# Kernel tuning notes

Measured on AMD Instinct MI355X. Metric: run time of the kernel, lower is better.

Reference implementation:

```python
import jax, jax.numpy as jnp
import numpy as np

N = 50000          # num nodes
E = 800000         # num edges (avg degree 16)
D_IN = 128         # input_size
H = 128            # hidden_size
BN_EPS = 1e-5


def setup_inputs() -> dict:
    key = jax.random.key(0)
    ks = jax.random.split(key, 16)
    std = 1.0 / np.sqrt(H)
    u = lambda k, shape: jax.random.uniform(k, shape, jnp.float32, -std, std)
    return {
        "x": jax.random.normal(ks[0], (N, D_IN), jnp.float32),
        "hx": jax.random.normal(ks[1], (N, H), jnp.float32),
        "cx": jax.random.normal(ks[2], (N, H), jnp.float32),
        "edge_src": jax.random.randint(ks[3], (E,), 0, N, jnp.int32),
        "edge_dst": jax.random.randint(ks[4], (E,), 0, N, jnp.int32),
        "edge_weight": jax.random.uniform(ks[5], (E,), jnp.float32) / 16.0,  # ~normalized adj values
        "gcn_weight": u(ks[6], (D_IN, H)),
        "bias": u(ks[7], (H,)),
        "x2h_w": u(ks[8], (4 * H, H)),
        "x2h_b": u(ks[9], (4 * H,)),
        "h2h_w": u(ks[10], (4 * H, H)),
        "h2h_b": u(ks[11], (4 * H,)),
        "bn_gamma": u(ks[12], (H,)),
        "bn_beta": u(ks[13], (H,)),
        "bn_mean": jnp.zeros((H,), jnp.float32),
        "bn_var": jnp.ones((H,), jnp.float32),
    }


def reference(x, hx, cx, edge_src, edge_dst, edge_weight, gcn_weight, bias,
              x2h_w, x2h_b, h2h_w, h2h_b, bn_gamma, bn_beta, bn_mean, bn_var):
    # GCN: support = x @ W, then sparse adj @ support via gather/segment-sum
    support = x @ gcn_weight                                   # (N, H)
    msgs = edge_weight[:, None] * support[edge_src]            # (E, H)
    agg = jax.ops.segment_sum(msgs, edge_dst, num_segments=N)  # (N, H) = spmm(adj, support)
    h = jax.nn.relu(agg)
    # dropout: eval mode -> identity
    h = h + bias
    # BatchNorm1d (eval mode, running stats)
    h = (h - bn_mean) * jax.lax.rsqrt(bn_var + BN_EPS) * bn_gamma + bn_beta
    # fused LSTM gates: x2h(h) + h2h(hx)
    gates = h @ x2h_w.T + x2h_b + hx @ h2h_w.T + h2h_b         # (N, 4H)
    i_g, f_g, g_g, o_g = jnp.split(gates, 4, axis=1)
    cy = cx * jax.nn.sigmoid(f_g) + jax.nn.sigmoid(i_g) * jnp.tanh(g_g)
    hy = jax.nn.sigmoid(o_g) * jnp.tanh(cy)
    return hy, cy
```

## Files before the change

kernel.cpp:

```cpp
#include <hip/hip_runtime.h>

#define NN 50000
#define NE 800000
#define HH 128
#define BN_EPS 1e-5f
#define SCAN_NB ((NN + 255) / 256)

typedef unsigned short u16;
typedef unsigned int u32;
typedef short bf16x8 __attribute__((ext_vector_type(8)));
typedef float f32x4 __attribute__((ext_vector_type(4)));

static __device__ __forceinline__ float bf2f(u16 u){
  union { u32 i; float f; } v; v.i = ((u32)u) << 16; return v.f;
}
static __device__ __forceinline__ u16 f2bf(float f){
  union { float f; u32 i; } v; v.f = f;
  u32 x = v.i;
  return (u16)((x + 0x7fffu + ((x >> 16) & 1u)) >> 16);
}
static __device__ __forceinline__ float sigm(float x){
  return 1.f / (1.f + __expf(-x));
}
static __device__ __forceinline__ float tanh_fast(float x){
  return 1.f - 2.f / (1.f + __expf(2.f * x));
}


__global__ void zero_kernel(int* __restrict__ p, int n){
  int i = blockIdx.x * blockDim.x + threadIdx.x;
  if (i < n) p[i] = 0;
}

__global__ void hist_kernel(const int* __restrict__ dst, int* __restrict__ counts, int E){
  int e = blockIdx.x * blockDim.x + threadIdx.x;
  if (e < E) atomicAdd(&counts[dst[e]], 1);
}


__global__ __launch_bounds__(256) void scan_bsum(
    const int* __restrict__ counts, int* __restrict__ bsums, int n){
  int i = blockIdx.x * 256 + threadIdx.x;
  int v = (i < n) ? counts[i] : 0;
#pragma unroll
  for (int off = 1; off < 64; off <<= 1) v += __shfl_xor(v, off);
  __shared__ int ws[4];
  if ((threadIdx.x & 63) == 0) ws[threadIdx.x >> 6] = v;
  __syncthreads();
  if (threadIdx.x == 0) bsums[blockIdx.x] = ws[0] + ws[1] + ws[2] + ws[3];
}

__global__ __launch_bounds__(256) void scan_tops(int* __restrict__ bsums, int nb){
  __shared__ int sh[256];
  int t = threadIdx.x;
  int v = (t < nb) ? bsums[t] : 0;
  sh[t] = v;
  __syncthreads();
  for (int off = 1; off < 256; off <<= 1){
    int u = (t >= off) ? sh[t - off] : 0;
    __syncthreads();
    sh[t] += u;
    __syncthreads();
  }
  if (t < nb) bsums[t] = sh[t] - v;
}

__global__ __launch_bounds__(256) void scan_final(
    const int* __restrict__ counts, const int* __restrict__ bsums,
    int* __restrict__ offs, int* __restrict__ cursor, int n){
  __shared__ int sh[256];
  int t = threadIdx.x;
  int i = blockIdx.x * 256 + t;
  int v = (i < n) ? counts[i] : 0;
  sh[t] = v;
  __syncthreads();
  for (int off = 1; off < 256; off <<= 1){
    int u = (t >= off) ? sh[t - off] : 0;
    __syncthreads();
    sh[t] += u;
    __syncthreads();
  }
  int excl = sh[t] - v + bsums[blockIdx.x];
  if (i < n){ offs[i] = excl; cursor[i] = excl; }
}

__global__ void scatter_kernel(const int* __restrict__ src, const int* __restrict__ dst,
                               const float* __restrict__ w, int* __restrict__ cursor,
                               int2* __restrict__ esw, int E){
  int e = blockIdx.x * blockDim.x + threadIdx.x;
  if (e < E){
    int d = dst[e];
    int pos = atomicAdd(&cursor[d], 1);
    esw[pos] = make_int2(src[e], __float_as_int(w[e]));
  }
}


__global__ void prep_pack(const float* __restrict__ x2hw, const float* __restrict__ h2hw,
                          const float* __restrict__ x2hb, const float* __restrict__ h2hb,
                          const float* __restrict__ gcnw,
                          u16* __restrict__ wcat, u16* __restrict__ wgcn,
                          float* __restrict__ bsum){
  int i = blockIdx.x * blockDim.x + threadIdx.x;
  int n = i >> 8, k = i & 255;
  float v = (k < 128) ? x2hw[n * 128 + k] : h2hw[n * 128 + (k - 128)];
  wcat[i] = f2bf(v);
  if (i < 16384){
    int nn = i >> 7, kk = i & 127;
    wgcn[i] = f2bf(gcnw[kk * 128 + nn]);
  }
  if (i < 512) bsum[i] = x2hb[i] + h2hb[i];
}

__global__ __launch_bounds__(256) void support_mfma(
    const float* __restrict__ x, const u16* __restrict__ wgcn,
    u16* __restrict__ support, int N){
  int tid = threadIdx.x;
  int wave = tid >> 6, lane = tid & 63;
  int c = lane & 15, q = lane >> 4;
  int row0 = blockIdx.x * 64 + wave * 16;
  int arow = row0 + c; if (arow > N - 1) arow = N - 1;
  f32x4 acc[8];
#pragma unroll
  for (int t = 0; t < 8; t++) acc[t] = (f32x4){0.f, 0.f, 0.f, 0.f};

  const u16* wp = wgcn + (size_t)c * 128 + q * 8;
#pragma unroll
  for (int k0 = 0; k0 < 128; k0 += 32){
    const float* ap = x + (size_t)arow * 128 + k0 + q * 8;
    float4 f0 = *(const float4*)ap;
    float4 f1 = *(const float4*)(ap + 4);
    u16 tmp[8] = {f2bf(f0.x), f2bf(f0.y), f2bf(f0.z), f2bf(f0.w),
                  f2bf(f1.x), f2bf(f1.y), f2bf(f1.z), f2bf(f1.w)};
    bf16x8 afrag = *(bf16x8*)tmp;
#pragma unroll
    for (int t = 0; t < 8; t++){
      bf16x8 bfrag = *(const bf16x8*)(wp + (size_t)t * 16 * 128 + k0);
      acc[t] = __builtin_amdgcn_mfma_f32_16x16x32_bf16(afrag, bfrag, acc[t], 0, 0, 0);
    }
  }
#pragma unroll
  for (int t = 0; t < 8; t++){
#pragma unroll
    for (int j = 0; j < 4; j++){
      int r = row0 + q * 4 + j;
      if (r < N) support[(size_t)r * 128 + t * 16 + c] = f2bf(acc[t][j]);
    }
  }
}

__global__ __launch_bounds__(256) void agg_bn2(
    const u16* __restrict__ support, const int2* __restrict__ esw,
    const int* __restrict__ offs, const int* __restrict__ counts,
    const float* __restrict__ bias, const float* __restrict__ gamma,
    const float* __restrict__ beta, const float* __restrict__ mean,
    const float* __restrict__ var, const float* __restrict__ hx,
    u16* __restrict__ hbn, u16* __restrict__ hxb, int N){
  int wid = blockIdx.x * 4 + (threadIdx.x >> 6);
  int lane = threadIdx.x & 63;
  if (wid >= N) return;
  int c = lane * 2;
  float2 hv = *(const float2*)(hx + (size_t)wid * HH + c);
  int start = offs[wid];
  int deg   = counts[wid];
  float a0 = 0.f, a1 = 0.f;
  for (int base = 0; base < deg; base += 64){
    int cnt = deg - base; if (cnt > 64) cnt = 64;
    int2 my = make_int2(0, 0);
    if (lane < cnt) my = esw[start + base + lane];
    int e = 0;
    for (; e + 8 <= cnt; e += 8){
      int s[8]; float g[8]; u32 u[8];
#pragma unroll
      for (int k = 0; k < 8; k++){
        s[k] = __shfl(my.x, e + k);
        g[k] = __int_as_float(__shfl(my.y, e + k));
      }
#pragma unroll
      for (int k = 0; k < 8; k++)
        u[k] = *(const u32*)(support + (size_t)s[k] * HH + c);
#pragma unroll
      for (int k = 0; k < 8; k++){
        a0 = fmaf(g[k], bf2f((u16)(u[k] & 0xffffu)), a0);
        a1 = fmaf(g[k], bf2f((u16)(u[k] >> 16)), a1);
      }
    }
    for (; e + 4 <= cnt; e += 4){
      int s[4]; float g[4]; u32 u[4];
#pragma unroll
      for (int k = 0; k < 4; k++){
        s[k] = __shfl(my.x, e + k);
        g[k] = __int_as_float(__shfl(my.y, e + k));
      }
#pragma unroll
      for (int k = 0; k < 4; k++)
        u[k] = *(const u32*)(support + (size_t)s[k] * HH + c);
#pragma unroll
      for (int k = 0; k < 4; k++){
        a0 = fmaf(g[k], bf2f((u16)(u[k] & 0xffffu)), a0);
        a1 = fmaf(g[k], bf2f((u16)(u[k] >> 16)), a1);
      }
    }
    for (; e < cnt; e++){
      int   si = __shfl(my.x, e);
      float gi = __int_as_float(__shfl(my.y, e));
      u32 ui = *(const u32*)(support + (size_t)si * HH + c);
      a0 = fmaf(gi, bf2f((u16)(ui & 0xffffu)), a0);
      a1 = fmaf(gi, bf2f((u16)(ui >> 16)), a1);
    }
  }
  float h0 = fmaxf(a0, 0.f) + bias[c];
  float h1 = fmaxf(a1, 0.f) + bias[c + 1];
  float s0 = gamma[c]     * rsqrtf(var[c]     + BN_EPS);
  float s1 = gamma[c + 1] * rsqrtf(var[c + 1] + BN_EPS);
  float r0 = (h0 - mean[c])     * s0 + beta[c];
  float r1 = (h1 - mean[c + 1]) * s1 + beta[c + 1];
  u32 pack = (u32)f2bf(r0) | ((u32)f2bf(r1) << 16);
  *(u32*)(hbn + (size_t)wid * HH + c) = pack;
  u32 hp = (u32)f2bf(hv.x) | ((u32)f2bf(hv.y) << 16);
  *(u32*)(hxb + (size_t)wid * HH + c) = hp;
}

__global__ __launch_bounds__(256, 4) void gates_mfma3(
    const u16* __restrict__ hbn, const u16* __restrict__ hxb,
    const u16* __restrict__ wcat, const float* __restrict__ bsum,
    const float* __restrict__ cx, float* __restrict__ out, int N){
  __shared__ bf16x8 lds_b[2048];
  int tid = threadIdx.x;
  int wave = tid >> 6, lane = tid & 63;
  int c = lane & 15, q = lane >> 4;
  int hg = blockIdx.y;
  int hloc = hg * 16 + c;

#pragma unroll
  for (int i = 0; i < 8; i++){
    int idx = i * 256 + tid;
    int f = idx >> 6, l = idx & 63;
    int g = f >> 3, kk = f & 7;
    int lq = l >> 4, lc = l & 15;
    const u16* src = wcat + (size_t)(g * 128 + hg * 16 + lc) * 256 + kk * 32 + lq * 8;
    lds_b[idx] = *(const bf16x8*)src;
  }
  __syncthreads();

  float bi  = bsum[hloc];
  float bf_ = bsum[128 + hloc];
  float bg  = bsum[256 + hloc];
  float bo  = bsum[384 + hloc];
  const size_t NH = (size_t)N * HH;

  const int nchunk = (N + 127) >> 7;
  for (int chunk = blockIdx.x; chunk < nchunk; chunk += gridDim.x){
    int rowbase = chunk * 128 + wave * 32;
    f32x4 acc[2][4];
#pragma unroll
    for (int b = 0; b < 2; b++)
#pragma unroll
      for (int g = 0; g < 4; g++) acc[b][g] = (f32x4){0.f, 0.f, 0.f, 0.f};
    int ar0 = rowbase + c;      if (ar0 > N - 1) ar0 = N - 1;
    int ar1 = rowbase + 16 + c; if (ar1 > N - 1) ar1 = N - 1;

#pragma unroll
    for (int kk = 0; kk < 8; kk++){
      const u16* abase = ((kk < 4) ? (hbn + (size_t)(kk * 32))
                                   : (hxb + (size_t)((kk - 4) * 32))) + q * 8;
      bf16x8 a0 = *(const bf16x8*)(abase + (size_t)ar0 * 128);
      bf16x8 a1 = *(const bf16x8*)(abase + (size_t)ar1 * 128);
#pragma unroll
      for (int g = 0; g < 4; g++){
        bf16x8 bfrag = lds_b[(g * 8 + kk) * 64 + lane];
        acc[0][g] = __builtin_amdgcn_mfma_f32_16x16x32_bf16(a0, bfrag, acc[0][g], 0, 0, 0);
        acc[1][g] = __builtin_amdgcn_mfma_f32_16x16x32_bf16(a1, bfrag, acc[1][g], 0, 0, 0);
      }
    }
#pragma unroll
    for (int b = 0; b < 2; b++){
#pragma unroll
      for (int j = 0; j < 4; j++){
        int r = rowbase + b * 16 + q * 4 + j;
        if (r < N){
          float gi = acc[b][0][j] + bi;
          float gf = acc[b][1][j] + bf_;
          float gg = acc[b][2][j] + bg;
          float go = acc[b][3][j] + bo;
          float is = sigm(gi), fs = sigm(gf), gt = tanh_fast(gg), os = sigm(go);
          float co = cx[(size_t)r * HH + hloc];
          float cyv = co * fs + is * gt;
          out[(size_t)r * HH + hloc]      = os * tanh_fast(cyv);
          out[NH + (size_t)r * HH + hloc] = cyv;
        }
      }
    }
  }
}


extern "C" void kernel_launch(void* const* d_in, const int* in_sizes, int n_in,
                              void* d_out, int out_size, void* d_ws, size_t ws_size,
                              hipStream_t stream){
  const float* x     = (const float*)d_in[0];
  const float* hx    = (const float*)d_in[1];
  const float* cx    = (const float*)d_in[2];
  const int*   esrc  = (const int*)d_in[3];
  const int*   edst  = (const int*)d_in[4];
  const float* ew    = (const float*)d_in[5];
  const float* gcn_w = (const float*)d_in[6];
  const float* bias  = (const float*)d_in[7];
  const float* x2hw  = (const float*)d_in[8];
  const float* x2hb  = (const float*)d_in[9];
  const float* h2hw  = (const float*)d_in[10];
  const float* h2hb  = (const float*)d_in[11];
  const float* bn_g  = (const float*)d_in[12];
  const float* bn_b  = (const float*)d_in[13];
  const float* bn_m  = (const float*)d_in[14];
  const float* bn_v  = (const float*)d_in[15];
  float* out = (float*)d_out;

  char* w = (char*)d_ws;
  u16* support = (u16*)w; w += (((size_t)NN * HH * 2) + 255) & ~(size_t)255;
  u16* hbn     = (u16*)w; w += (((size_t)NN * HH * 2) + 255) & ~(size_t)255;
  u16* hxb     = (u16*)w; w += (((size_t)NN * HH * 2) + 255) & ~(size_t)255;
  int* counts  = (int*)w; w += (((size_t)NN * 4) + 255) & ~(size_t)255;
  int* offs    = (int*)w; w += (((size_t)NN * 4) + 255) & ~(size_t)255;
  int* cursor  = (int*)w; w += (((size_t)NN * 4) + 255) & ~(size_t)255;
  int* bsums   = (int*)w; w += (((size_t)SCAN_NB * 4) + 255) & ~(size_t)255;
  int2* esw    = (int2*)w; w += (((size_t)NE * 8) + 255) & ~(size_t)255;
  u16* wcat    = (u16*)w; w += (((size_t)512 * 256 * 2) + 255) & ~(size_t)255;
  u16* wgcn    = (u16*)w; w += (((size_t)128 * 128 * 2) + 255) & ~(size_t)255;
  float* bsum  = (float*)w; w += (((size_t)512 * 4) + 255) & ~(size_t)255;

  prep_pack<<<512, 256, 0, stream>>>(x2hw, h2hw, x2hb, h2hb, gcn_w, wcat, wgcn, bsum);
  zero_kernel<<<(NN + 255) / 256, 256, 0, stream>>>(counts, NN);
  hist_kernel<<<(NE + 255) / 256, 256, 0, stream>>>(edst, counts, NE);
  scan_bsum<<<SCAN_NB, 256, 0, stream>>>(counts, bsums, NN);
  scan_tops<<<1, 256, 0, stream>>>(bsums, SCAN_NB);
  scan_final<<<SCAN_NB, 256, 0, stream>>>(counts, bsums, offs, cursor, NN);
  scatter_kernel<<<(NE + 255) / 256, 256, 0, stream>>>(esrc, edst, ew, cursor, esw, NE);
  support_mfma<<<(NN + 63) / 64, 256, 0, stream>>>(x, wgcn, support, NN);
  agg_bn2<<<(NN + 3) / 4, 256, 0, stream>>>(support, esw, offs, counts,
                                            bias, bn_g, bn_b, bn_m, bn_v, hx, hbn, hxb, NN);
  gates_mfma3<<<dim3(128, 8), 256, 0, stream>>>(hbn, hxb, wcat, bsum, cx, out, NN);
}
```

Baseline: 408.8 us.

## Widen gates kernel to 1024-thread blocks covering 64 hidden columns with pre-swizzled weights

```diff
diff --git a/kernel.cpp b/kernel.cpp
--- a/kernel.cpp
+++ b/kernel.cpp
@@ -95,7 +95,6 @@
   }
 }
 
-
 __global__ void prep_pack(const float* __restrict__ x2hw, const float* __restrict__ h2hw,
                           const float* __restrict__ x2hb, const float* __restrict__ h2hb,
                           const float* __restrict__ gcnw,
@@ -104,10 +103,12 @@
   int i = blockIdx.x * blockDim.x + threadIdx.x;
   int n = i >> 8, k = i & 255;
   float v = (k < 128) ? x2hw[n * 128 + k] : h2hw[n * 128 + (k - 128)];
-  wcat[i] = f2bf(v);
+  int nt = n >> 4, lc = n & 15;
+  int kk = k >> 5, lq = (k >> 3) & 3, e = k & 7;
+  wcat[(((nt * 8 + kk) * 64) + lq * 16 + lc) * 8 + e] = f2bf(v);
   if (i < 16384){
-    int nn = i >> 7, kk = i & 127;
-    wgcn[i] = f2bf(gcnw[kk * 128 + nn]);
+    int nn = i >> 7, kx = i & 127;
+    wgcn[i] = f2bf(gcnw[kx * 128 + nn]);
   }
   if (i < 512) bsum[i] = x2hb[i] + h2hb[i];
 }
@@ -221,25 +222,26 @@
   *(u32*)(hxb + (size_t)wid * HH + c) = hp;
 }
 
-__global__ __launch_bounds__(256, 4) void gates_mfma3(
+__global__ __launch_bounds__(1024) void gates_mfma4(
     const u16* __restrict__ hbn, const u16* __restrict__ hxb,
     const u16* __restrict__ wcat, const float* __restrict__ bsum,
     const float* __restrict__ cx, float* __restrict__ out, int N){
-  __shared__ bf16x8 lds_b[2048];
+  __shared__ bf16x8 lds_b[8192];
   int tid = threadIdx.x;
   int wave = tid >> 6, lane = tid & 63;
   int c = lane & 15, q = lane >> 4;
-  int hg = blockIdx.y;
-  int hloc = hg * 16 + c;
-
-#pragma unroll
-  for (int i = 0; i < 8; i++){
-    int idx = i * 256 + tid;
-    int f = idx >> 6, l = idx & 63;
-    int g = f >> 3, kk = f & 7;
-    int lq = l >> 4, lc = l & 15;
-    const u16* src = wcat + (size_t)(g * 128 + hg * 16 + lc) * 256 + kk * 32 + lq * 8;
-    lds_b[idx] = *(const bf16x8*)src;
+  int rb = wave >> 2, cg = wave & 3;
+  int hc = blockIdx.y;
+  int hloc = hc * 64 + cg * 16 + c;
+
+  const bf16x8* wsrc = (const bf16x8*)wcat;
+#pragma unroll
+  for (int it = 0; it < 8; it++){
+    int idx = it * 1024 + tid;
+    int lf = idx >> 6, l = idx & 63;
+    int scg = lf >> 5, sg = (lf >> 3) & 3, skk = lf & 7;
+    int nt = sg * 8 + hc * 4 + scg;
+    lds_b[idx] = wsrc[(nt * 8 + skk) * 64 + l];
   }
   __syncthreads();
 
@@ -251,7 +253,7 @@
 
   const int nchunk = (N + 127) >> 7;
   for (int chunk = blockIdx.x; chunk < nchunk; chunk += gridDim.x){
-    int rowbase = chunk * 128 + wave * 32;
+    int rowbase = chunk * 128 + rb * 32;
     f32x4 acc[2][4];
 #pragma unroll
     for (int b = 0; b < 2; b++)
@@ -268,7 +270,7 @@
       bf16x8 a1 = *(const bf16x8*)(abase + (size_t)ar1 * 128);
 #pragma unroll
       for (int g = 0; g < 4; g++){
-        bf16x8 bfrag = lds_b[(g * 8 + kk) * 64 + lane];
+        bf16x8 bfrag = lds_b[((cg * 4 + g) * 8 + kk) * 64 + lane];
         acc[0][g] = __builtin_amdgcn_mfma_f32_16x16x32_bf16(a0, bfrag, acc[0][g], 0, 0, 0);
         acc[1][g] = __builtin_amdgcn_mfma_f32_16x16x32_bf16(a1, bfrag, acc[1][g], 0, 0, 0);
       }
@@ -339,5 +341,5 @@
   support_mfma<<<(NN + 63) / 64, 256, 0, stream>>>(x, wgcn, support, NN);
   agg_bn2<<<(NN + 3) / 4, 256, 0, stream>>>(support, esw, offs, counts,
                                             bias, bn_g, bn_b, bn_m, bn_v, hx, hbn, hxb, NN);
-  gates_mfma3<<<dim3(128, 8), 256, 0, stream>>>(hbn, hxb, wcat, bsum, cx, out, NN);
-}
+  gates_mfma4<<<dim3(128, 2), 1024, 0, stream>>>(hbn, hxb, wcat, bsum, cx, out, NN);
+}
```

Measured after the change: 404.1 us. Within noise of the previous version (-1.1%).
